# Kernel optimization log

Hardware: AMD Instinct MI355X
Metric: run time of the kernel (lower is better)

The kernel has to match this reference:

```python
import jax, jax.numpy as jnp
import numpy as np

N = 40000      # nodes
E = 400000     # edges
G = 64         # graphs in batch
IN = 128       # input feature dim
D = 64         # num_hidden (per-head out dim)
H = 4          # heads per layer
C = 10         # num_classes
SLOPE = 0.2    # leaky_relu negative slope


def setup_inputs() -> dict:
    key = jax.random.key(0)
    ks = jax.random.split(key, 16)

    def p(k, shape, fan):
        return jax.random.normal(k, shape, jnp.float32) * (1.0 / np.sqrt(fan))

    x = jax.random.normal(ks[0], (N, IN), jnp.float32)
    src = jax.random.randint(ks[1], (E,), 0, N, dtype=jnp.int32)
    dst = jax.random.randint(ks[2], (E,), 0, N, dtype=jnp.int32)
    graph_id = jnp.sort(jax.random.randint(ks[3], (N,), 0, G, dtype=jnp.int32))

    W0 = p(ks[4], (IN, H * D), IN)
    al0 = p(ks[5], (H, D), D)
    ar0 = p(ks[6], (H, D), D)
    W1 = p(ks[7], (H * D, H * D), H * D)
    al1 = p(ks[8], (H, D), D)
    ar1 = p(ks[9], (H, D), D)
    W2 = p(ks[10], (H * D, H * D), H * D)
    al2 = p(ks[11], (H, D), D)
    ar2 = p(ks[12], (H, D), D)
    Wc = p(ks[13], (D, C), D)
    bc = jnp.zeros((C,), jnp.float32)
    return dict(x=x, src=src, dst=dst, graph_id=graph_id,
                W0=W0, al0=al0, ar0=ar0, W1=W1, al1=al1, ar1=ar1,
                W2=W2, al2=al2, ar2=ar2, Wc=Wc, bc=bc)


def gat_layer(h, W, al, ar, src, dst, residual, activate):
    # DGL GATConv (no bias): project, per-edge attention, edge-softmax, aggregate.
    n = h.shape[0]
    Hh, Dd = al.shape
    feat = (h @ W).reshape(n, Hh, Dd)                       # [N,H,D]
    el = jnp.einsum('nhd,hd->nh', feat, al)                 # [N,H]
    er = jnp.einsum('nhd,hd->nh', feat, ar)                 # [N,H]
    e = jax.nn.leaky_relu(el[src] + er[dst], SLOPE)         # [E,H]
    # numerically stable edge softmax over incoming edges of each dst node
    m = jax.ops.segment_max(e, dst, num_segments=n)
    m = jnp.where(jnp.isfinite(m), m, 0.0)                  # isolated nodes -> -inf
    ee = jnp.exp(e - m[dst])                                # [E,H]
    denom = jax.ops.segment_sum(ee, dst, num_segments=n)
    alpha = ee / jnp.maximum(denom[dst], 1e-9)              # [E,H]
    msg = feat[src] * alpha[..., None]                      # [E,H,D]
    out = jax.ops.segment_sum(msg, dst, num_segments=n)     # [N,H,D]
    if residual:  # identity residual (in == H*D)
        out = out + h.reshape(n, Hh, Dd)
    if activate:
        out = jax.nn.elu(out)
    return out


def reference(x, src, dst, graph_id, W0, al0, ar0, W1, al1, ar1,
              W2, al2, ar2, Wc, bc):
    h = gat_layer(x, W0, al0, ar0, src, dst, False, True).reshape(N, H * D)
    h = gat_layer(h, W1, al1, ar1, src, dst, True, True).reshape(N, H * D)
    h = gat_layer(h, W2, al2, ar2, src, dst, True, False).mean(axis=1)  # [N,D]
    # mean_nodes readout over batched graphs
    cnt = jax.ops.segment_sum(jnp.ones((N,), jnp.float32), graph_id, num_segments=G)
    hg = jax.ops.segment_sum(h, graph_id, num_segments=G) / jnp.maximum(cnt, 1.0)[:, None]
    return hg @ Wc + bc                                     # [G,C]
```

## Files before the change

kernel.cpp:

```cpp
#include <hip/hip_runtime.h>
#include <hip/hip_bf16.h>
#include <math.h>

#define N_NODES 40000
#define N_EDGES 400000
#define N_GRAPH 64
#define IN_DIM 128
#define HD 256
#define NCLS 10
#define SLOPE 0.2f

typedef __hip_bfloat16 bf16;
typedef __attribute__((ext_vector_type(8))) short short8;
typedef __attribute__((ext_vector_type(4))) float floatx4;

__device__ __forceinline__ float b2f(bf16 x){ return __bfloat162float(x); }
__device__ __forceinline__ bf16  f2b(float x){ return __float2bfloat16(x); }

__device__ __forceinline__ floatx4 unpack4(uint2 u){
  floatx4 f;
  f[0] = __uint_as_float(u.x << 16);
  f[1] = __uint_as_float(u.x & 0xffff0000u);
  f[2] = __uint_as_float(u.y << 16);
  f[3] = __uint_as_float(u.y & 0xffff0000u);
  return f;
}

__device__ __forceinline__ int wave_incl_scan(int x, int lane){
  #pragma unroll
  for (int m=1;m<64;m<<=1){
    int v = __shfl_up(x, m);
    if (lane >= m) x += v;
  }
  return x;
}

__global__ __launch_bounds__(256) void prep_kernel(const float4* __restrict__ x4, ushort* __restrict__ xc,
                                                   const float* __restrict__ W0, ushort* __restrict__ Wt0,
                                                   const float* __restrict__ W1, ushort* __restrict__ Wt1,
                                                   const float* __restrict__ W2, ushort* __restrict__ Wt2,
                                                   int* __restrict__ cnt, float* __restrict__ gacc)
{
  int b = blockIdx.x, t = threadIdx.x;
  if (b < 5000){
    int i = b*256 + t;
    float4 v = x4[i];
    ushort4 o;
    o.x = __bfloat16_as_ushort(f2b(v.x));
    o.y = __bfloat16_as_ushort(f2b(v.y));
    o.z = __bfloat16_as_ushort(f2b(v.z));
    o.w = __bfloat16_as_ushort(f2b(v.w));
    *(ushort4*)(xc + i*4) = o;
  } else if (b < 5640){
    const float* W; ushort* Wt; int e0, n_el;
    if (b < 5128){ W = W0; Wt = Wt0; e0 = (b-5000)*256; n_el = IN_DIM*HD; }
    else if (b < 5384){ W = W1; Wt = Wt1; e0 = (b-5128)*256; n_el = HD*HD; }
    else { W = W2; Wt = Wt2; e0 = (b-5384)*256; n_el = HD*HD; }
    int e = e0 + t;
    if (e < n_el){
      int k = e >> 8, n = e & 255;
      int idx = (((k>>6)*256 + n)<<6) + (k & 63);
      Wt[idx] = __bfloat16_as_ushort(f2b(W[e]));
    }
  } else if (b < 5797){
    int i = (b-5640)*256 + t;
    if (i < N_NODES) cnt[i] = 0;
  } else {
    #pragma unroll
    for (int k=0;k<16;++k) gacc[t*16 + k] = 0.f;
  }
}

__global__ __launch_bounds__(256) void hist_kernel(const int* __restrict__ dst, int* __restrict__ cnt){
  int i = blockIdx.x*256 + threadIdx.x;
  if (i < N_EDGES) atomicAdd(&cnt[dst[i]], 1);
}

__global__ __launch_bounds__(1024) void reduce_kernel(const int* __restrict__ cnt, int* __restrict__ bsum){
  int t = threadIdx.x, b = blockIdx.x;
  int idx = b*1024 + t;
  int c = (idx < N_NODES) ? cnt[idx] : 0;
  #pragma unroll
  for (int m=32;m;m>>=1) c += __shfl_down(c, m);
  __shared__ int ws[16];
  int w = t>>6, l = t&63;
  if (l==0) ws[w] = c;
  __syncthreads();
  if (t==0){
    int s = 0;
    #pragma unroll
    for (int i=0;i<16;i++) s += ws[i];
    bsum[b] = s;
  }
}

__global__ __launch_bounds__(1024) void csr_scan_kernel(const int* __restrict__ cnt, const int* __restrict__ bsum,
                                                        int* __restrict__ rs, int* __restrict__ cur){
  int t = threadIdx.x, b = blockIdx.x;
  __shared__ int boff_s;
  if (t < 64){
    int v = (t < 40) ? bsum[t] : 0;
    int incl = wave_incl_scan(v, t);
    if (t == b) boff_s = incl - v;
    if (b == 39 && t == 39) rs[N_NODES] = incl;
  }
  int idx = b*1024 + t;
  int c = (idx < N_NODES) ? cnt[idx] : 0;
  int w = t>>6, l = t&63;
  int wi = wave_incl_scan(c, l);
  __shared__ int ws[16];
  __shared__ int wexcl[16];
  if (l==63) ws[w] = wi;
  __syncthreads();
  if (t < 16){
    int x = ws[t];
    #pragma unroll
    for (int m=1;m<16;m<<=1){
      int v = __shfl_up(x, m);
      if (t >= m) x += v;
    }
    wexcl[t] = x - ws[t];
  }
  __syncthreads();
  if (idx < N_NODES){
    int p = boff_s + wexcl[w] + wi - c;
    rs[idx] = p; cur[idx] = p;
  }
}

__global__ __launch_bounds__(256) void scatter_kernel(const int* __restrict__ src, const int* __restrict__ dst,
                                                      int* __restrict__ cur, int* __restrict__ csrc){
  int i = blockIdx.x*256 + threadIdx.x;
  if (i < N_EDGES){
    int p = atomicAdd(&cur[dst[i]], 1);
    csrc[p] = src[i];
  }
}

template<int K>
__global__ __launch_bounds__(256) void gemm_kernel(const bf16* __restrict__ A, const ushort* __restrict__ Wt,
                                                   bf16* __restrict__ C,
                                                   const float* __restrict__ al, const float* __restrict__ ar,
                                                   float* __restrict__ el, float* __restrict__ er)
{
  __shared__ __align__(16) short As[64][72];
  int t = threadIdx.x;
  int lane = t & 63, w = t >> 6;
  int quad = lane >> 4, l15 = lane & 15;
  int bm = blockIdx.x;
  const ushort* Au = (const ushort*)A;
  floatx4 acc[4][4] = {};
  int srow = t >> 3, scol = (t & 7) << 3;

  for (int kc = 0; kc < K/64; ++kc){
    __syncthreads();
    #pragma unroll
    for (int i=0;i<2;++i){
      int row = srow + 32*i;
      short8 v = *(const short8*)(Au + (size_t)(bm*64 + row)*K + kc*64 + scol);
      *(short8*)&As[row][scol] = v;
    }
    __syncthreads();
    #pragma unroll
    for (int j=0;j<2;++j){
      short8 af[4], bfr[4];
      #pragma unroll
      for (int mt=0;mt<4;++mt) af[mt] = *(const short8*)&As[16*mt + l15][8*quad + 32*j];
      #pragma unroll
      for (int ct=0;ct<4;++ct){
        int n = w*64 + 16*ct + l15;
        bfr[ct] = *(const short8*)(Wt + ((size_t)(kc*256 + n)<<6) + 8*quad + 32*j);
      }
      #pragma unroll
      for (int mt=0;mt<4;++mt)
        #pragma unroll
        for (int ct=0;ct<4;++ct)
          acc[mt][ct] = __builtin_amdgcn_mfma_f32_16x16x32_bf16(af[mt], bfr[ct], acc[mt][ct], 0, 0, 0);
    }
  }

  #pragma unroll
  for (int mt=0;mt<4;++mt)
    #pragma unroll
    for (int ct=0;ct<4;++ct)
      #pragma unroll
      for (int r=0;r<4;++r){
        int row = bm*64 + 16*mt + 4*quad + r;
        C[(size_t)row*HD + w*64 + 16*ct + l15] = f2b(acc[mt][ct][r]);
      }

  float alv[4], arv[4];
  #pragma unroll
  for (int ct=0;ct<4;++ct){ alv[ct] = al[w*64 + 16*ct + l15]; arv[ct] = ar[w*64 + 16*ct + l15]; }
  #pragma unroll
  for (int mt=0;mt<4;++mt)
    #pragma unroll
    for (int r=0;r<4;++r){
      float pe = 0.f, pr_ = 0.f;
      #pragma unroll
      for (int ct=0;ct<4;++ct){ float v = acc[mt][ct][r]; pe += v*alv[ct]; pr_ += v*arv[ct]; }
      #pragma unroll
      for (int m=1;m<16;m<<=1){ pe += __shfl_xor(pe, m); pr_ += __shfl_xor(pr_, m); }
      if (l15 == 0){
        int row = bm*64 + 16*mt + 4*quad + r;
        el[row*4 + w] = pe;
        er[row*4 + w] = pr_;
      }
    }
}

__global__ __launch_bounds__(256) void agg_kernel(const bf16* __restrict__ feat,
                                                  const float* __restrict__ el, const float* __restrict__ er,
                                                  const int* __restrict__ rs, const int* __restrict__ csrc,
                                                  bf16* __restrict__ h_io,
                                                  int residual, int activate)
{
  int t = threadIdx.x;
  int w = t >> 6, l = t & 63;
  int n = blockIdx.x*4 + w;
  int h = l >> 4;
  float er_h = er[n*4 + h];
  int j0 = rs[n], j1 = rs[n+1];
  const uint2* fp = (const uint2*)feat;
  uint2* hp = (uint2*)h_io;

  floatx4 res = {0,0,0,0};
  if (residual) res = unpack4(hp[(size_t)n*64 + l]);

  floatx4 a0={0,0,0,0}, a1={0,0,0,0}, a2={0,0,0,0}, a3={0,0,0,0};
  float d0=0.f, d1=0.f, d2=0.f, d3=0.f;

  for (int base = j0; base < j1; base += 64){
    int m = j1 - base; if (m > 64) m = 64;
    int eidx = csrc[base + (l < m ? l : m-1)];
    int jj = 0;
    for (; jj+3 < m; jj += 4){
      int s0 = __shfl(eidx, jj),   s1 = __shfl(eidx, jj+1);
      int s2 = __shfl(eidx, jj+2), s3 = __shfl(eidx, jj+3);
      float e0 = el[s0*4+h] + er_h;
      float e1 = el[s1*4+h] + er_h;
      float e2 = el[s2*4+h] + er_h;
      float e3 = el[s3*4+h] + er_h;
      e0 = (e0 > 0.f) ? e0 : SLOPE*e0;
      e1 = (e1 > 0.f) ? e1 : SLOPE*e1;
      e2 = (e2 > 0.f) ? e2 : SLOPE*e2;
      e3 = (e3 > 0.f) ? e3 : SLOPE*e3;
      float ee0 = __expf(e0), ee1 = __expf(e1), ee2 = __expf(e2), ee3 = __expf(e3);
      floatx4 f0 = unpack4(fp[(size_t)s0*64 + l]);
      floatx4 f1 = unpack4(fp[(size_t)s1*64 + l]);
      floatx4 f2 = unpack4(fp[(size_t)s2*64 + l]);
      floatx4 f3 = unpack4(fp[(size_t)s3*64 + l]);
      d0 += ee0; d1 += ee1; d2 += ee2; d3 += ee3;
      #pragma unroll
      for (int k=0;k<4;++k){
        a0[k] += ee0*f0[k]; a1[k] += ee1*f1[k];
        a2[k] += ee2*f2[k]; a3[k] += ee3*f3[k];
      }
    }
    for (; jj < m; ++jj){
      int s0 = __shfl(eidx, jj);
      float e0 = el[s0*4+h] + er_h;
      e0 = (e0 > 0.f) ? e0 : SLOPE*e0;
      float ee0 = __expf(e0);
      floatx4 f0 = unpack4(fp[(size_t)s0*64 + l]);
      d0 += ee0;
      #pragma unroll
      for (int k=0;k<4;++k) a0[k] += ee0*f0[k];
    }
  }
  float den = fmaxf((d0+d1)+(d2+d3), 1e-9f);
  ushort4 o;
  #pragma unroll
  for (int k=0;k<4;++k){
    float v = ((a0[k]+a1[k])+(a2[k]+a3[k])) / den + res[k];
    if (activate) v = (v > 0.f) ? v : expm1f(v);
    ((ushort*)&o)[k] = __bfloat16_as_ushort(f2b(v));
  }
  *(ushort4*)&hp[(size_t)n*64 + l] = o;
}

__global__ __launch_bounds__(256) void readout_kernel(const bf16* __restrict__ h2, const int* __restrict__ gid,
                                                      float* __restrict__ gacc)
{
  int t = threadIdx.x;
  int w = t >> 6, l = t & 63;
  int nbase = blockIdx.x*64 + w*16;
  const uint2* hp = (const uint2*)h2;
  floatx4 run = {0,0,0,0};
  int curg = gid[nbase];
  for (int i=0;i<16;++i){
    int n = nbase + i;
    int g = gid[n];
    floatx4 v = unpack4(hp[(size_t)n*64 + l]);
    #pragma unroll
    for (int k=0;k<4;++k){ v[k] += __shfl_xor(v[k], 16); v[k] += __shfl_xor(v[k], 32); v[k] *= 0.25f; }
    if (g != curg){
      if (l < 16){
        #pragma unroll
        for (int k=0;k<4;++k) atomicAdd(&gacc[curg*64 + 4*l + k], run[k]);
      }
      run = (floatx4){0,0,0,0}; curg = g;
    }
    if (l < 16){
      #pragma unroll
      for (int k=0;k<4;++k) run[k] += v[k];
    }
  }
  if (l < 16){
    #pragma unroll
    for (int k=0;k<4;++k) atomicAdd(&gacc[curg*64 + 4*l + k], run[k]);
  }
}

__global__ __launch_bounds__(64) void classifier_kernel(const float* __restrict__ gacc, const int* __restrict__ gid,
                                                        const float* __restrict__ Wc, const float* __restrict__ bc,
                                                        float* __restrict__ out)
{
  int g = blockIdx.x, d = threadIdx.x;
  __shared__ float hg[64];
  __shared__ int cnt_s;
  if (d == 0){
    int lo = 0, hi = N_NODES;
    while (lo < hi){ int mid = (lo+hi)>>1; if (gid[mid] < g) lo = mid+1; else hi = mid; }
    int start = lo;
    hi = N_NODES;
    while (lo < hi){ int mid = (lo+hi)>>1; if (gid[mid] <= g) lo = mid+1; else hi = mid; }
    cnt_s = lo - start;
  }
  hg[d] = gacc[g*64+d];
  __syncthreads();
  float inv = 1.0f / fmaxf((float)cnt_s, 1.0f);
  if (d < NCLS){
    float s = 0.f;
    #pragma unroll
    for (int k=0;k<64;k++) s += hg[k] * Wc[k*NCLS + d];
    out[g*NCLS + d] = bc[d] + s * inv;
  }
}

__global__ __launch_bounds__(64) void diag_kernel(float* __restrict__ out, float v){
  int i = blockIdx.x*64 + threadIdx.x;
  if (i < N_GRAPH*NCLS) out[i] = v;
}

#define WS_NEEDED 54589216ull

extern "C" void kernel_launch(void* const* d_in, const int* in_sizes, int n_in,
                              void* d_out, int out_size, void* d_ws, size_t ws_size,
                              hipStream_t stream)
{
  (void)out_size;
  float* out = (float*)d_out;

  if (ws_size < WS_NEEDED){
    diag_kernel<<<10, 64, 0, stream>>>(out, (float)(ws_size >> 20));
    return;
  }
  static const int sz_dict[15] = {5120000,400000,400000,40000,32768,256,256,65536,256,256,65536,256,256,640,10};
  bool okd = (n_in >= 15);
  if (okd) for (int i=0;i<15;i++) if (in_sizes[i] != sz_dict[i]) { okd = false; break; }
  if (!okd){ diag_kernel<<<10, 64, 0, stream>>>(out, 3.0f); return; }

  const float* x  = (const float*)d_in[0];
  const int* src  = (const int*)d_in[1];
  const int* dst  = (const int*)d_in[2];
  const int* gid  = (const int*)d_in[3];
  const float* W0 = (const float*)d_in[4];
  const float* al0= (const float*)d_in[5];
  const float* ar0= (const float*)d_in[6];
  const float* W1 = (const float*)d_in[7];
  const float* al1= (const float*)d_in[8];
  const float* ar1= (const float*)d_in[9];
  const float* W2 = (const float*)d_in[10];
  const float* al2= (const float*)d_in[11];
  const float* ar2= (const float*)d_in[12];
  const float* Wc = (const float*)d_in[13];
  const float* bc = (const float*)d_in[14];

  char* ws = (char*)d_ws;
  int*    rs   = (int*)   (ws + 256);
  int*    csrc = (int*)   (ws + 160512);
  float*  el   = (float*) (ws + 1760512);
  float*  er   = (float*) (ws + 2400512);
  int*    cnt  = (int*)   (ws + 1760512);
  int*    cur  = (int*)   (ws + 2400512);
  bf16*   H    = (bf16*)  (ws + 3040512);
  bf16*   feat = (bf16*)  (ws + 23520512);
  float*  gacc = (float*) (ws + 44000512);
  bf16*   xc   = (bf16*)  (ws + 44017152);
  ushort* Wt0  = (ushort*)(ws + 54257152);
  ushort* Wt1  = (ushort*)(ws + 54322688);
  ushort* Wt2  = (ushort*)(ws + 54453760);
  int*    bsum = (int*)   (ws + 54584832);

  prep_kernel<<<5798, 256, 0, stream>>>((const float4*)x, (ushort*)xc,
                                        W0, Wt0, W1, Wt1, W2, Wt2, cnt, gacc);

  const int eb = (N_EDGES + 255)/256;
  const int sb = (N_NODES + 1023)/1024;
  hist_kernel    <<<eb, 256, 0, stream>>>(dst, cnt);
  reduce_kernel  <<<sb, 1024, 0, stream>>>(cnt, bsum);
  csr_scan_kernel<<<sb, 1024, 0, stream>>>(cnt, bsum, rs, cur);
  scatter_kernel <<<eb, 256, 0, stream>>>(src, dst, cur, csrc);

  gemm_kernel<IN_DIM><<<625, 256, 0, stream>>>(xc, Wt0, feat, al0, ar0, el, er);
  agg_kernel<<<N_NODES/4, 256, 0, stream>>>(feat, el, er, rs, csrc, H, 0, 1);
  gemm_kernel<HD><<<625, 256, 0, stream>>>(H, Wt1, feat, al1, ar1, el, er);
  agg_kernel<<<N_NODES/4, 256, 0, stream>>>(feat, el, er, rs, csrc, H, 1, 1);
  gemm_kernel<HD><<<625, 256, 0, stream>>>(H, Wt2, feat, al2, ar2, el, er);
  agg_kernel<<<N_NODES/4, 256, 0, stream>>>(feat, el, er, rs, csrc, H, 1, 0);
  readout_kernel   <<<625, 256, 0, stream>>>(H, gid, gacc);
  classifier_kernel<<<N_GRAPH, 64, 0, stream>>>(gacc, gid, Wc, bc, out);
}
```

Before: 340.4 us.

## Fuse input conversion into GEMM, merge CSR scan passes, fold readout into aggregation

```diff
diff --git a/kernel.cpp b/kernel.cpp
--- a/kernel.cpp
+++ b/kernel.cpp
@@ -35,35 +35,25 @@
   return x;
 }
 
-__global__ __launch_bounds__(256) void prep_kernel(const float4* __restrict__ x4, ushort* __restrict__ xc,
-                                                   const float* __restrict__ W0, ushort* __restrict__ Wt0,
+__global__ __launch_bounds__(256) void prep_kernel(const float* __restrict__ W0, ushort* __restrict__ Wt0,
                                                    const float* __restrict__ W1, ushort* __restrict__ Wt1,
                                                    const float* __restrict__ W2, ushort* __restrict__ Wt2,
                                                    int* __restrict__ cnt, float* __restrict__ gacc)
 {
   int b = blockIdx.x, t = threadIdx.x;
-  if (b < 5000){
-    int i = b*256 + t;
-    float4 v = x4[i];
-    ushort4 o;
-    o.x = __bfloat16_as_ushort(f2b(v.x));
-    o.y = __bfloat16_as_ushort(f2b(v.y));
-    o.z = __bfloat16_as_ushort(f2b(v.z));
-    o.w = __bfloat16_as_ushort(f2b(v.w));
-    *(ushort4*)(xc + i*4) = o;
-  } else if (b < 5640){
+  if (b < 640){
     const float* W; ushort* Wt; int e0, n_el;
-    if (b < 5128){ W = W0; Wt = Wt0; e0 = (b-5000)*256; n_el = IN_DIM*HD; }
-    else if (b < 5384){ W = W1; Wt = Wt1; e0 = (b-5128)*256; n_el = HD*HD; }
-    else { W = W2; Wt = Wt2; e0 = (b-5384)*256; n_el = HD*HD; }
+    if (b < 128){ W = W0; Wt = Wt0; e0 = b*256; n_el = IN_DIM*HD; }
+    else if (b < 384){ W = W1; Wt = Wt1; e0 = (b-128)*256; n_el = HD*HD; }
+    else { W = W2; Wt = Wt2; e0 = (b-384)*256; n_el = HD*HD; }
     int e = e0 + t;
     if (e < n_el){
       int k = e >> 8, n = e & 255;
       int idx = (((k>>6)*256 + n)<<6) + (k & 63);
       Wt[idx] = __bfloat16_as_ushort(f2b(W[e]));
     }
-  } else if (b < 5797){
-    int i = (b-5640)*256 + t;
+  } else if (b < 797){
+    int i = (b-640)*256 + t;
     if (i < N_NODES) cnt[i] = 0;
   } else {
     #pragma unroll
@@ -76,37 +66,26 @@
   if (i < N_EDGES) atomicAdd(&cnt[dst[i]], 1);
 }
 
-__global__ __launch_bounds__(1024) void reduce_kernel(const int* __restrict__ cnt, int* __restrict__ bsum){
+__global__ __launch_bounds__(1024) void csr_scan_kernel(const int* __restrict__ cnt,
+                                                        int* __restrict__ rs, int* __restrict__ cur){
   int t = threadIdx.x, b = blockIdx.x;
+  int w = t>>6, l = t&63;
+  int pre = 0;
+  for (int i = t; i < b*1024; i += 1024) pre += cnt[i];
+  #pragma unroll
+  for (int m=32;m;m>>=1) pre += __shfl_down(pre, m);
+  __shared__ int pw[16];
+  if (l == 0) pw[w] = pre;
+  __syncthreads();
+  __shared__ int boff_s;
+  if (t == 0){
+    int s = 0;
+    #pragma unroll
+    for (int i=0;i<16;i++) s += pw[i];
+    boff_s = s;
+  }
   int idx = b*1024 + t;
   int c = (idx < N_NODES) ? cnt[idx] : 0;
-  #pragma unroll
-  for (int m=32;m;m>>=1) c += __shfl_down(c, m);
-  __shared__ int ws[16];
-  int w = t>>6, l = t&63;
-  if (l==0) ws[w] = c;
-  __syncthreads();
-  if (t==0){
-    int s = 0;
-    #pragma unroll
-    for (int i=0;i<16;i++) s += ws[i];
-    bsum[b] = s;
-  }
-}
-
-__global__ __launch_bounds__(1024) void csr_scan_kernel(const int* __restrict__ cnt, const int* __restrict__ bsum,
-                                                        int* __restrict__ rs, int* __restrict__ cur){
-  int t = threadIdx.x, b = blockIdx.x;
-  __shared__ int boff_s;
-  if (t < 64){
-    int v = (t < 40) ? bsum[t] : 0;
-    int incl = wave_incl_scan(v, t);
-    if (t == b) boff_s = incl - v;
-    if (b == 39 && t == 39) rs[N_NODES] = incl;
-  }
-  int idx = b*1024 + t;
-  int c = (idx < N_NODES) ? cnt[idx] : 0;
-  int w = t>>6, l = t&63;
   int wi = wave_incl_scan(c, l);
   __shared__ int ws[16];
   __shared__ int wexcl[16];
@@ -126,6 +105,7 @@
     int p = boff_s + wexcl[w] + wi - c;
     rs[idx] = p; cur[idx] = p;
   }
+  if (b == 39 && t == 0) rs[N_NODES] = N_EDGES;
 }
 
 __global__ __launch_bounds__(256) void scatter_kernel(const int* __restrict__ src, const int* __restrict__ dst,
@@ -137,8 +117,8 @@
   }
 }
 
-template<int K>
-__global__ __launch_bounds__(256) void gemm_kernel(const bf16* __restrict__ A, const ushort* __restrict__ Wt,
+template<int K, int AF32>
+__global__ __launch_bounds__(256) void gemm_kernel(const void* __restrict__ A, const ushort* __restrict__ Wt,
                                                    bf16* __restrict__ C,
                                                    const float* __restrict__ al, const float* __restrict__ ar,
                                                    float* __restrict__ el, float* __restrict__ er)
@@ -148,7 +128,6 @@
   int lane = t & 63, w = t >> 6;
   int quad = lane >> 4, l15 = lane & 15;
   int bm = blockIdx.x;
-  const ushort* Au = (const ushort*)A;
   floatx4 acc[4][4] = {};
   int srow = t >> 3, scol = (t & 7) << 3;
 
@@ -157,7 +136,20 @@
     #pragma unroll
     for (int i=0;i<2;++i){
       int row = srow + 32*i;
-      short8 v = *(const short8*)(Au + (size_t)(bm*64 + row)*K + kc*64 + scol);
+      short8 v;
+      if (AF32){
+        const float* Af = (const float*)A;
+        const float* p = Af + (size_t)(bm*64 + row)*K + kc*64 + scol;
+        float4 u0 = *(const float4*)p;
+        float4 u1 = *(const float4*)(p + 4);
+        v[0]=(short)__bfloat16_as_ushort(f2b(u0.x)); v[1]=(short)__bfloat16_as_ushort(f2b(u0.y));
+        v[2]=(short)__bfloat16_as_ushort(f2b(u0.z)); v[3]=(short)__bfloat16_as_ushort(f2b(u0.w));
+        v[4]=(short)__bfloat16_as_ushort(f2b(u1.x)); v[5]=(short)__bfloat16_as_ushort(f2b(u1.y));
+        v[6]=(short)__bfloat16_as_ushort(f2b(u1.z)); v[7]=(short)__bfloat16_as_ushort(f2b(u1.w));
+      } else {
+        const ushort* Au = (const ushort*)A;
+        v = *(const short8*)(Au + (size_t)(bm*64 + row)*K + kc*64 + scol);
+      }
       *(short8*)&As[row][scol] = v;
     }
     __syncthreads();
@@ -213,7 +205,8 @@
                                                   const float* __restrict__ el, const float* __restrict__ er,
                                                   const int* __restrict__ rs, const int* __restrict__ csrc,
                                                   bf16* __restrict__ h_io,
-                                                  int residual, int activate)
+                                                  const int* __restrict__ gid, float* __restrict__ gacc,
+                                                  int mode)
 {
   int t = threadIdx.x;
   int w = t >> 6, l = t & 63;
@@ -225,7 +218,7 @@
   uint2* hp = (uint2*)h_io;
 
   floatx4 res = {0,0,0,0};
-  if (residual) res = unpack4(hp[(size_t)n*64 + l]);
+  if (mode >= 1) res = unpack4(hp[(size_t)n*64 + l]);
 
   floatx4 a0={0,0,0,0}, a1={0,0,0,0}, a2={0,0,0,0}, a3={0,0,0,0};
   float d0=0.f, d1=0.f, d2=0.f, d3=0.f;
@@ -269,46 +262,30 @@
     }
   }
   float den = fmaxf((d0+d1)+(d2+d3), 1e-9f);
-  ushort4 o;
-  #pragma unroll
-  for (int k=0;k<4;++k){
-    float v = ((a0[k]+a1[k])+(a2[k]+a3[k])) / den + res[k];
-    if (activate) v = (v > 0.f) ? v : expm1f(v);
-    ((ushort*)&o)[k] = __bfloat16_as_ushort(f2b(v));
-  }
-  *(ushort4*)&hp[(size_t)n*64 + l] = o;
-}
-
-__global__ __launch_bounds__(256) void readout_kernel(const bf16* __restrict__ h2, const int* __restrict__ gid,
-                                                      float* __restrict__ gacc)
-{
-  int t = threadIdx.x;
-  int w = t >> 6, l = t & 63;
-  int nbase = blockIdx.x*64 + w*16;
-  const uint2* hp = (const uint2*)h2;
-  floatx4 run = {0,0,0,0};
-  int curg = gid[nbase];
-  for (int i=0;i<16;++i){
-    int n = nbase + i;
+
+  if (mode == 2){
+    floatx4 v;
+    #pragma unroll
+    for (int k=0;k<4;++k){
+      v[k] = ((a0[k]+a1[k])+(a2[k]+a3[k])) / den + res[k];
+      v[k] += __shfl_xor(v[k], 16);
+      v[k] += __shfl_xor(v[k], 32);
+      v[k] *= 0.25f;
+    }
     int g = gid[n];
-    floatx4 v = unpack4(hp[(size_t)n*64 + l]);
-    #pragma unroll
-    for (int k=0;k<4;++k){ v[k] += __shfl_xor(v[k], 16); v[k] += __shfl_xor(v[k], 32); v[k] *= 0.25f; }
-    if (g != curg){
-      if (l < 16){
-        #pragma unroll
-        for (int k=0;k<4;++k) atomicAdd(&gacc[curg*64 + 4*l + k], run[k]);
-      }
-      run = (floatx4){0,0,0,0}; curg = g;
-    }
     if (l < 16){
       #pragma unroll
-      for (int k=0;k<4;++k) run[k] += v[k];
-    }
-  }
-  if (l < 16){
-    #pragma unroll
-    for (int k=0;k<4;++k) atomicAdd(&gacc[curg*64 + 4*l + k], run[k]);
+      for (int k=0;k<4;++k) atomicAdd(&gacc[g*64 + 4*l + k], v[k]);
+    }
+  } else {
+    ushort4 o;
+    #pragma unroll
+    for (int k=0;k<4;++k){
+      float v = ((a0[k]+a1[k])+(a2[k]+a3[k])) / den + res[k];
+      v = (v > 0.f) ? v : expm1f(v);
+      ((ushort*)&o)[k] = __bfloat16_as_ushort(f2b(v));
+    }
+    *(ushort4*)&hp[(size_t)n*64 + l] = o;
   }
 }
 
@@ -387,28 +364,22 @@
   bf16*   H    = (bf16*)  (ws + 3040512);
   bf16*   feat = (bf16*)  (ws + 23520512);
   float*  gacc = (float*) (ws + 44000512);
-  bf16*   xc   = (bf16*)  (ws + 44017152);
   ushort* Wt0  = (ushort*)(ws + 54257152);
   ushort* Wt1  = (ushort*)(ws + 54322688);
   ushort* Wt2  = (ushort*)(ws + 54453760);
-  int*    bsum = (int*)   (ws + 54584832);
-
-  prep_kernel<<<5798, 256, 0, stream>>>((const float4*)x, (ushort*)xc,
-                                        W0, Wt0, W1, Wt1, W2, Wt2, cnt, gacc);
+
+  prep_kernel<<<798, 256, 0, stream>>>(W0, Wt0, W1, Wt1, W2, Wt2, cnt, gacc);
 
   const int eb = (N_EDGES + 255)/256;
-  const int sb = (N_NODES + 1023)/1024;
   hist_kernel    <<<eb, 256, 0, stream>>>(dst, cnt);
-  reduce_kernel  <<<sb, 1024, 0, stream>>>(cnt, bsum);
-  csr_scan_kernel<<<sb, 1024, 0, stream>>>(cnt, bsum, rs, cur);
+  csr_scan_kernel<<<40, 1024, 0, stream>>>(cnt, rs, cur);
   scatter_kernel <<<eb, 256, 0, stream>>>(src, dst, cur, csrc);
 
-  gemm_kernel<IN_DIM><<<625, 256, 0, stream>>>(xc, Wt0, feat, al0, ar0, el, er);
-  agg_kernel<<<N_NODES/4, 256, 0, stream>>>(feat, el, er, rs, csrc, H, 0, 1);
-  gemm_kernel<HD><<<625, 256, 0, stream>>>(H, Wt1, feat, al1, ar1, el, er);
-  agg_kernel<<<N_NODES/4, 256, 0, stream>>>(feat, el, er, rs, csrc, H, 1, 1);
-  gemm_kernel<HD><<<625, 256, 0, stream>>>(H, Wt2, feat, al2, ar2, el, er);
-  agg_kernel<<<N_NODES/4, 256, 0, stream>>>(feat, el, er, rs, csrc, H, 1, 0);
-  readout_kernel   <<<625, 256, 0, stream>>>(H, gid, gacc);
+  gemm_kernel<IN_DIM,1><<<625, 256, 0, stream>>>(x, Wt0, feat, al0, ar0, el, er);
+  agg_kernel<<<N_NODES/4, 256, 0, stream>>>(feat, el, er, rs, csrc, H, gid, gacc, 0);
+  gemm_kernel<HD,0><<<625, 256, 0, stream>>>(H, Wt1, feat, al1, ar1, el, er);
+  agg_kernel<<<N_NODES/4, 256, 0, stream>>>(feat, el, er, rs, csrc, H, gid, gacc, 1);
+  gemm_kernel<HD,0><<<625, 256, 0, stream>>>(H, Wt2, feat, al2, ar2, el, er);
+  agg_kernel<<<N_NODES/4, 256, 0, stream>>>(feat, el, er, rs, csrc, H, gid, gacc, 2);
   classifier_kernel<<<N_GRAPH, 64, 0, stream>>>(gacc, gid, Wc, bc, out);
 }
```

Result: slower. 484.3 us (+42.3%).
